# Kernel tuning notes

Measured on AMD Instinct MI355X. Metric: run time of the kernel, lower is better.

## Reference

```python
import jax, jax.numpy as jnp
import numpy as np

B, C, L, M, EMB, HID = 32, 64, 8192, 32, 256, 64

def setup_inputs() -> dict:
    key = jax.random.key(0)
    ks = jax.random.split(key, 14)
    s_w = 1.0 / (C * C)
    s_a = 1.0 / EMB
    return {
        "x": jax.random.normal(ks[0], (B, C, L), jnp.float32),
        "emb": jax.random.normal(ks[1], (B, EMB), jnp.float32),
        "weights_pos": s_w * jax.random.normal(ks[2], (C, C, M, 2), jnp.float32),
        "weights_neg": s_w * jax.random.normal(ks[3], (C, C, M, 2), jnp.float32),
        "A_real_pos": s_a * jax.random.normal(ks[4], (M, EMB), jnp.float32),
        "A_imag_pos": s_a * jax.random.normal(ks[5], (M, EMB), jnp.float32),
        "A_real_neg": s_a * jax.random.normal(ks[6], (M, EMB), jnp.float32),
        "A_imag_neg": s_a * jax.random.normal(ks[7], (M, EMB), jnp.float32),
        "tm_w1": 0.05 * jax.random.normal(ks[8], (HID, EMB), jnp.float32),
        "tm_b1": jnp.zeros((HID,), jnp.float32),
        "tm_w2": 0.05 * jax.random.normal(ks[9], (2 * C, HID), jnp.float32),
        "tm_b2": jnp.zeros((2 * C,), jnp.float32),
        "lin_w": 0.05 * jax.random.normal(ks[10], (C, C), jnp.float32),
        "lin_b": jnp.zeros((C,), jnp.float32),
    }

def reference(x, emb, weights_pos, weights_neg, A_real_pos, A_imag_pos,
              A_real_neg, A_imag_neg, tm_w1, tm_b1, tm_w2, tm_b2, lin_w, lin_b):
    b, c, l = x.shape
    m = weights_pos.shape[2]
    k = l // 2 + 1
    # ---- SpectralConv1d branch ----
    x_ft = jnp.fft.rfft(x, norm="ortho")  # [B,C,K] complex
    wp = weights_pos[..., 0] + 1j * weights_pos[..., 1]  # [Ci,Co,M]
    wn = weights_neg[..., 0] + 1j * weights_neg[..., 1]
    phi_p = (emb @ A_real_pos.T) + 1j * (emb @ A_imag_pos.T)  # [B,M]
    phi_n = (emb @ A_real_neg.T) + 1j * (emb @ A_imag_neg.T)
    out_pos = jnp.einsum("bim,iom->bom", x_ft[:, :, :m], wp) * phi_p[:, None, :]
    out_neg = jnp.einsum("bim,iom->bom", x_ft[:, :, k - m:], wn) * phi_n[:, None, :]
    out_ft = jnp.zeros((b, c, k), dtype=x_ft.dtype)
    out_ft = out_ft.at[:, :, :m].set(out_pos).at[:, :, k - m:].set(out_neg)
    x1 = jnp.fft.irfft(out_ft, n=l, norm="ortho")  # [B,C,L]
    # ---- Conv1DTime branch (FiLM-style) ----
    h = jax.nn.silu(emb @ tm_w1.T + tm_b1)          # [B,HID]
    gb = h @ tm_w2.T + tm_b2                         # [B,2C]
    gamma, beta = gb[:, :c], gb[:, c:]
    xl = jnp.einsum("bcl,oc->bol", x, lin_w) + lin_b[None, :, None]
    x2 = xl * (1.0 + gamma[:, :, None]) + beta[:, :, None]
    return jax.nn.silu(x1 + x2)
```

## Files before the change

### kernel.cpp

```cpp
#include <hip/hip_runtime.h>
#include <math.h>

#define L_ 8192
#define EMB_ 256
#define HID_ 64

typedef __attribute__((ext_vector_type(8))) short bf16x8;
typedef __attribute__((ext_vector_type(4))) float f32x4;
typedef __attribute__((ext_vector_type(4))) int i32x4;

#define OFF_TFB  0
#define OFF_TLB  262144
#define OFF_AFB  524288
#define OFF_XFRP 917504
#define OFF_B2   3014656
#define OFF_PHI  3016704
#define OFF_GB   3020800

__device__ inline int pkbf(float a, float b) {
    int r;
    asm volatile("v_cvt_pk_bf16_f32 %0, %1, %2" : "=v"(r) : "v"(a), "v"(b));
    return r;
}
__device__ inline bf16x8 asbf(i32x4 v) { union { i32x4 i; bf16x8 h; } u; u.i = v; return u.h; }
#define MFMA(A,B,C) __builtin_amdgcn_mfma_f32_16x16x32_bf16((A),(B),(C),0,0,0)

__device__ inline ushort f2bf(float v) {
    unsigned b = __float_as_uint(v);
    return (ushort)((b + 0x7FFFu + ((b >> 16) & 1u)) >> 16);
}
__device__ inline float bf2f(ushort h) { return __uint_as_float(((unsigned)h) << 16); }
__device__ inline float hwsin(float rev) { float r; asm("v_sin_f32 %0, %1" : "=v"(r) : "v"(rev)); return r; }
__device__ inline float hwcos(float rev) { float r; asm("v_cos_f32 %0, %1" : "=v"(r) : "v"(rev)); return r; }

__global__ __launch_bounds__(256) void k_init(ushort* __restrict__ TLB, ushort* __restrict__ TFB,
        const float* __restrict__ emb,
        const float* __restrict__ Arp, const float* __restrict__ Aip,
        const float* __restrict__ Arn, const float* __restrict__ Ain, float* __restrict__ phi,
        const float* __restrict__ w1, const float* __restrict__ b1,
        const float* __restrict__ w2, const float* __restrict__ b2, float* __restrict__ gb) {
    int bid = blockIdx.x;
    if (bid < 4096) {
        int idx = bid * 256 + threadIdx.x;
        int f, l; ushort* dst;
        if (idx < 524288) {
            int u = idx;
            int e = u & 7, lane = (u >> 3) & 63, ct = (u >> 9) & 3, kstep = u >> 11;
            l = kstep * 32 + ((lane >> 4) << 3) + e;
            f = ct * 16 + (lane & 15);
            dst = TLB + u;
        } else {
            int u = idx - 524288;
            int e = u & 7, lane = (u >> 3) & 63, ts = (u >> 9) & 1, lt = u >> 10;
            l = lt * 16 + (lane & 15);
            f = ts * 32 + ((lane >> 4) << 3) + e;
            dst = TFB + u;
        }
        int fr = f & 31; bool sinp = (f & 32) != 0;
        int r = (fr * l) & (L_ - 1);
        float rev = (float)r * (1.0f / (float)L_);
        float v = sinp ? hwsin(rev) : hwcos(rev);
        *dst = f2bf(v);
    } else if (bid < 4112) {
        int tid = (bid - 4096) * 256 + threadIdx.x;
        int b = tid >> 7;
        int mm = (tid >> 2) & 31;
        int cmp = tid & 3;
        const float* A = (cmp == 0) ? Arp : (cmp == 1) ? Aip : (cmp == 2) ? Arn : Ain;
        const float4* e4 = (const float4*)(emb + b * EMB_);
        const float4* a4 = (const float4*)(A + mm * EMB_);
        float acc = 0.f;
        for (int q = 0; q < EMB_ / 4; ++q) {
            float4 ev = e4[q], av = a4[q];
            acc += ev.x * av.x + ev.y * av.y + ev.z * av.z + ev.w * av.w;
        }
        phi[tid] = acc;
    } else {
        __shared__ float h[HID_];
        int b = bid - 4112, t = threadIdx.x;
        if (t < HID_) {
            const float4* e4 = (const float4*)(emb + b * EMB_);
            const float4* w4 = (const float4*)(w1 + t * EMB_);
            float acc = b1[t];
            for (int q = 0; q < EMB_ / 4; ++q) {
                float4 ev = e4[q], wv = w4[q];
                acc += ev.x * wv.x + ev.y * wv.y + ev.z * wv.z + ev.w * wv.w;
            }
            h[t] = acc / (1.f + expf(-acc));
        }
        __syncthreads();
        if (t < 128) {
            float g = b2[t];
            const float4* h4 = (const float4*)h;
            const float4* w4 = (const float4*)(w2 + t * HID_);
            for (int q = 0; q < HID_ / 4; ++q) {
                float4 hv = h4[q], wv = w4[q];
                g += hv.x * wv.x + hv.y * wv.y + hv.z * wv.z + hv.w * wv.w;
            }
            if (t < 64) gb[(b * 64 + t) * 2 + 0] = 1.f + g;
            else        gb[(b * 64 + (t - 64)) * 2 + 1] = g;
        }
    }
}

__global__ __launch_bounds__(256) void k_dft(const float* __restrict__ x,
        const ushort* __restrict__ TLB, float* __restrict__ xfrp) {
    __shared__ float sP[4][16][132];
    int stripe = blockIdx.x >> 3;
    int lseg = blockIdx.x & 7;
    int w = threadIdx.x >> 6;
    int lane = threadIdx.x & 63;
    int row = lane & 15, koff = (lane >> 4) << 3;
    int r0 = stripe * 16;
    int kb0 = lseg * 1024 + w * 256;

    f32x4 acc[8];
    #pragma unroll
    for (int i = 0; i < 8; ++i) acc[i] = (f32x4){0.f, 0.f, 0.f, 0.f};

    const float* ap = x + (size_t)(r0 + row) * L_ + kb0 + koff;
    const i32x4* tb = (const i32x4*)TLB;
    int tbase = (kb0 >> 5) * 256 + lane;
    const i32x4 SM = {(int)0x80000000, (int)0x80000000, (int)0x80000000, (int)0x80000000};

    float4 xa0 = *(const float4*)(ap);
    float4 xc0 = *(const float4*)(ap + 4);
    float4 xa1 = *(const float4*)(ap + 32);
    float4 xc1 = *(const float4*)(ap + 36);
    float4 xa2 = *(const float4*)(ap + 64);
    float4 xc2 = *(const float4*)(ap + 68);
    i32x4 t0 = tb[tbase], t1 = tb[tbase + 64], t2 = tb[tbase + 128], t3 = tb[tbase + 192];
    for (int ks = 0; ks < 8; ++ks) {
        float4 nxa = {0,0,0,0}, nxc = {0,0,0,0};
        i32x4 n0 = t0, n1 = t1, n2 = t2, n3 = t3;
        if (ks < 5) {
            nxa = *(const float4*)(ap + (ks + 3) * 32);
            nxc = *(const float4*)(ap + (ks + 3) * 32 + 4);
        }
        if (ks < 7) {
            int ti = tbase + (ks + 1) * 256;
            n0 = tb[ti]; n1 = tb[ti + 64]; n2 = tb[ti + 128]; n3 = tb[ti + 192];
        }
        int h0 = pkbf(xa0.x, xa0.y), h1 = pkbf(xa0.z, xa0.w);
        int h2 = pkbf(xc0.x, xc0.y), h3 = pkbf(xc0.z, xc0.w);
        bf16x8 AH = asbf((i32x4){h0, h1, h2, h3});
        acc[0] = MFMA(AH, asbf(t0), acc[0]); acc[4] = MFMA(AH, asbf(t0 ^ SM), acc[4]);
        acc[1] = MFMA(AH, asbf(t1), acc[1]); acc[5] = MFMA(AH, asbf(t1 ^ SM), acc[5]);
        acc[2] = MFMA(AH, asbf(t2), acc[2]); acc[6] = MFMA(AH, asbf(t2 ^ SM), acc[6]);
        acc[3] = MFMA(AH, asbf(t3), acc[3]); acc[7] = MFMA(AH, asbf(t3 ^ SM), acc[7]);
        xa0 = xa1; xc0 = xc1; xa1 = xa2; xc1 = xc2; xa2 = nxa; xc2 = nxc;
        t0 = n0; t1 = n1; t2 = n2; t3 = n3;
    }
    int crow = (lane >> 4) << 2;
    int ccol = lane & 15;
    #pragma unroll
    for (int ct = 0; ct < 8; ++ct)
        #pragma unroll
        for (int r = 0; r < 4; ++r)
            sP[w][crow + r][ct * 16 + ccol] = acc[ct][r];
    __syncthreads();
    #pragma unroll
    for (int i = 0; i < 8; ++i) {
        int e = threadIdx.x + 256 * i;
        int rr = e & 15, cc = e >> 4;
        float s = sP[0][rr][cc] + sP[1][rr][cc] + sP[2][rr][cc] + sP[3][rr][cc];
        xfrp[((size_t)(lseg * 128 + cc)) * 2048 + r0 + rr] = s;
    }
}

__global__ __launch_bounds__(256) void k_mix(const float* __restrict__ xfrt,
        const float* __restrict__ wpos, const float* __restrict__ wneg,
        const float* __restrict__ phi, const float* __restrict__ lw,
        const float* __restrict__ lb, const float* __restrict__ gb,
        ushort* __restrict__ afb, float* __restrict__ bias2) {
    int bi = blockIdx.x;
    int tid = threadIdx.x;
    if (bi >= 128) {
        int b = bi - 128;
        ushort* dst = afb + (size_t)b * 24576;
        #pragma unroll
        for (int j = 0; j < 16; ++j) {
            int u = tid + 256 * j;
            int e = u & 7, lane = (u >> 3) & 63, mt = (u >> 9) & 3, ks2 = u >> 11;
            int c = mt * 16 + (lane & 15);
            int kk = ((lane >> 4) << 3) + e;
            float v = lw[c * 64 + ks2 * 32 + kk] * gb[(b * 64 + c) * 2];
            ushort hi = f2bf(v);
            int base = (((4 + ks2) * 4 + mt) * 64 + lane) * 16;
            dst[base + e] = hi;
            dst[base + 8 + e] = f2bf(v - bf2f(hi));
        }
        if (tid < 64) {
            float g1 = gb[(b * 64 + tid) * 2], be = gb[(b * 64 + tid) * 2 + 1];
            bias2[b * 64 + tid] = lb[tid] * g1 + be;
        }
        return;
    }
    __shared__ float sW[64][64][2];
    __shared__ float sXr[16][64], sXi[16][64];
    int bh = bi & 1, side = (bi >> 1) & 1, mm = bi >> 2;
    int slot = side ? (31 - mm) : mm;
    int colR = side ? (64 + slot) : mm;
    int colI = side ? (96 + slot) : (32 + mm);

    const float* W = side ? wneg : wpos;
    #pragma unroll
    for (int j = 0; j < 16; ++j) {
        int fidx = tid + 256 * j;
        int i = fidx >> 6, o = fidx & 63;
        float2 wv = *(const float2*)&W[(size_t)(i * 64 + o) * 64 + mm * 2];
        sW[i][o][0] = wv.x;
        sW[i][o][1] = wv.y;
    }
    {
        const float4* pR = (const float4*)(xfrt + (size_t)colR * 2048 + bh * 1024);
        const float4* pI = (const float4*)(xfrt + (size_t)colI * 2048 + bh * 1024);
        float4 aR = {0, 0, 0, 0}, aI = {0, 0, 0, 0};
        #pragma unroll
        for (int s = 0; s < 8; ++s) {
            float4 vR = pR[(size_t)s * 65536 + tid];
            float4 vI = pI[(size_t)s * 65536 + tid];
            aR.x += vR.x; aR.y += vR.y; aR.z += vR.z; aR.w += vR.w;
            aI.x += vI.x; aI.y += vI.y; aI.z += vI.z; aI.w += vI.w;
        }
        if (!side) { aI.x = -aI.x; aI.y = -aI.y; aI.z = -aI.z; aI.w = -aI.w; }
        *(float4*)&sXr[tid >> 4][(tid & 15) * 4] = aR;
        *(float4*)&sXi[tid >> 4][(tid & 15) * 4] = aI;
    }
    __syncthreads();

    int o = tid & 63, bg = tid >> 6;
    const float invL = 1.f / (float)L_;
    float fac = (slot == 0) ? invL : 2.f * invL;
    int comp = side ? 2 : 0;
    int e = slot & 7, kgrp = slot >> 3;
    int mt = o >> 4, lane = kgrp * 16 + (o & 15);
    #pragma unroll
    for (int bl = 0; bl < 4; ++bl) {
        int b_local = bg * 4 + bl;
        int b = bh * 16 + b_local;
        float sre = 0.f, sim = 0.f;
        #pragma unroll 16
        for (int i = 0; i < 64; ++i) {
            float wr = sW[i][o][0], wi = sW[i][o][1];
            float xr = sXr[b_local][i], xi = sXi[b_local][i];
            sre += xr * wr - xi * wi;
            sim += xr * wi + xi * wr;
        }
        const float* ph = &phi[(b * 32 + mm) * 4 + (side ? 2 : 0)];
        float phr = ph[0], phim = ph[1];
        float Pre = sre * phr - sim * phim;
        float Pim = sre * phim + sim * phr;
        float a = fac * Pre;
        float bcoef = (slot == 0) ? 0.f : (side ? 2.f * invL * Pim : -2.f * invL * Pim);
        ushort* dst = afb + (size_t)b * 24576;
        ushort hiA = f2bf(a);
        int baseA = ((comp * 4 + mt) * 64 + lane) * 16;
        dst[baseA + e] = hiA;
        dst[baseA + 8 + e] = f2bf(a - bf2f(hiA));
        ushort hiB = f2bf(bcoef);
        int baseB = (((comp + 1) * 4 + mt) * 64 + lane) * 16;
        dst[baseB + e] = hiB;
        dst[baseB + 8 + e] = f2bf(bcoef - bf2f(hiB));
    }
}

__global__ __launch_bounds__(256, 4) void k_fuse(const float* __restrict__ x,
        const ushort* __restrict__ TFB, const ushort* __restrict__ AFB,
        const float* __restrict__ bias2, float* __restrict__ out) {
    int b = blockIdx.x >> 6, lt = blockIdx.x & 63;
    int w = threadIdx.x >> 6, lane = threadIdx.x & 63;
    int col = lane & 15, kgrp = lane >> 4;
    int lbase = lt * 128 + w * 32;
    int lt0 = lbase >> 4;
    const i32x4* tb = (const i32x4*)TFB;
    const i32x4* ab = (const i32x4*)AFB + (size_t)b * 3072;

    f32x4 acc[4][2];
    #pragma unroll
    for (int i = 0; i < 4; ++i)
        #pragma unroll
        for (int j = 0; j < 2; ++j) acc[i][j] = (f32x4){0.f, 0.f, 0.f, 0.f};

    int sm = (col & 1) ? (int)0x80008000 : 0;
    i32x4 SM = {sm, sm, sm, sm};

    auto tpart = [&](int ts) {
        i32x4 bh[2];
        #pragma unroll
        for (int nj = 0; nj < 2; ++nj)
            bh[nj] = tb[((lt0 + nj) * 2 + ts) * 64 + lane];
        #pragma unroll
        for (int mt = 0; mt < 4; ++mt) {
            i32x4 ah0 = ab[((ts * 4 + mt) * 64 + lane) * 2];
            i32x4 ah1 = ab[(((2 + ts) * 4 + mt) * 64 + lane) * 2];
            bf16x8 AH0 = asbf(ah0), AH1 = asbf(ah1);
            #pragma unroll
            for (int nj = 0; nj < 2; ++nj) {
                acc[mt][nj] = MFMA(AH0, asbf(bh[nj]), acc[mt][nj]);
                acc[mt][nj] = MFMA(AH1, asbf(bh[nj] ^ SM), acc[mt][nj]);
            }
        }
    };
    auto xissue = [&](int ts, float xv[2][8]) {
        #pragma unroll
        for (int nj = 0; nj < 2; ++nj) {
            const float* xp = x + (size_t)(b * 64 + ts * 32 + kgrp * 8) * L_ + lbase + nj * 16 + col;
            #pragma unroll
            for (int e = 0; e < 8; ++e) xv[nj][e] = xp[(size_t)e * L_];
        }
    };
    auto xpart = [&](int ts, float xv[2][8]) {
        #pragma unroll
        for (int nj = 0; nj < 2; ++nj) {
            int h0 = pkbf(xv[nj][0], xv[nj][1]), h1 = pkbf(xv[nj][2], xv[nj][3]);
            int h2 = pkbf(xv[nj][4], xv[nj][5]), h3 = pkbf(xv[nj][6], xv[nj][7]);
            bf16x8 XH = asbf((i32x4){h0, h1, h2, h3});
            #pragma unroll
            for (int mt = 0; mt < 4; ++mt) {
                i32x4 ah = ab[(((4 + ts) * 4 + mt) * 64 + lane) * 2];
                acc[mt][nj] = MFMA(asbf(ah), XH, acc[mt][nj]);
            }
        }
    };

    float xva[2][8], xvb[2][8];
    xissue(0, xva);
    tpart(0);
    xissue(1, xvb);
    xpart(0, xva);
    tpart(1);
    xpart(1, xvb);

    #pragma unroll
    for (int mt = 0; mt < 4; ++mt) {
        #pragma unroll
        for (int r = 0; r < 4; ++r) {
            int c = mt * 16 + kgrp * 4 + r;
            float bias = bias2[b * 64 + c];
            float* op = out + (size_t)(b * 64 + c) * L_ + lbase + col;
            #pragma unroll
            for (int nj = 0; nj < 2; ++nj) {
                float v = acc[mt][nj][r] + bias;
                op[nj * 16] = v / (1.f + __expf(-v));
            }
        }
    }
}

extern "C" void kernel_launch(void* const* d_in, const int* in_sizes, int n_in,
                              void* d_out, int out_size, void* d_ws, size_t ws_size,
                              hipStream_t stream) {
    const float* x    = (const float*)d_in[0];
    const float* emb  = (const float*)d_in[1];
    const float* wpos = (const float*)d_in[2];
    const float* wneg = (const float*)d_in[3];
    const float* Arp  = (const float*)d_in[4];
    const float* Aip  = (const float*)d_in[5];
    const float* Arn  = (const float*)d_in[6];
    const float* Ain  = (const float*)d_in[7];
    const float* w1   = (const float*)d_in[8];
    const float* b1   = (const float*)d_in[9];
    const float* w2   = (const float*)d_in[10];
    const float* b2   = (const float*)d_in[11];
    const float* lw   = (const float*)d_in[12];
    const float* lb   = (const float*)d_in[13];
    float* out = (float*)d_out;
    float* ws = (float*)d_ws;
    ushort* TFB  = (ushort*)(ws + OFF_TFB);
    ushort* TLB  = (ushort*)(ws + OFF_TLB);
    ushort* AFB  = (ushort*)(ws + OFF_AFB);
    float*  XFRP = ws + OFF_XFRP;
    float*  B2   = ws + OFF_B2;
    float*  PHI  = ws + OFF_PHI;
    float*  GB   = ws + OFF_GB;

    hipLaunchKernelGGL(k_init,  dim3(4144), dim3(256), 0, stream,
                       TLB, TFB, emb, Arp, Aip, Arn, Ain, PHI, w1, b1, w2, b2, GB);
    hipLaunchKernelGGL(k_dft,   dim3(1024), dim3(256), 0, stream, x, TLB, XFRP);
    hipLaunchKernelGGL(k_mix,   dim3(160),  dim3(256), 0, stream, XFRP, wpos, wneg, PHI,
                       lw, lb, GB, AFB, B2);
    hipLaunchKernelGGL(k_fuse,  dim3(2048), dim3(256), 0, stream, x, TFB, AFB, B2, out);
}
```

Measured before the change: 72.82 us.

## Split k_mix batch across more blocks, unroll DFT loop, reorder fuse x loads

k_mix now splits the batch into four groups of 8 instead of two groups of 16, so it launches 256 mixing blocks plus 32 affine blocks instead of 128 plus 32. This gives more parallelism on a small-grid kernel at the cost of reloading the weight tile in more blocks. The k_dft k-step loop is fully unrolled. In k_fuse the lambdas become macros, both x loads are issued before any MFMA work, and the occupancy hint drops from 4 to 3 blocks per CU to allow more registers for the earlier prefetch.

```diff
diff --git a/kernel.cpp b/kernel.cpp
--- a/kernel.cpp
+++ b/kernel.cpp
@@ -130,6 +130,7 @@
     float4 xa2 = *(const float4*)(ap + 64);
     float4 xc2 = *(const float4*)(ap + 68);
     i32x4 t0 = tb[tbase], t1 = tb[tbase + 64], t2 = tb[tbase + 128], t3 = tb[tbase + 192];
+    #pragma unroll
     for (int ks = 0; ks < 8; ++ks) {
         float4 nxa = {0,0,0,0}, nxc = {0,0,0,0};
         i32x4 n0 = t0, n1 = t1, n2 = t2, n3 = t3;
@@ -175,8 +176,8 @@
         ushort* __restrict__ afb, float* __restrict__ bias2) {
     int bi = blockIdx.x;
     int tid = threadIdx.x;
-    if (bi >= 128) {
-        int b = bi - 128;
+    if (bi >= 256) {
+        int b = bi - 256;
         ushort* dst = afb + (size_t)b * 24576;
         #pragma unroll
         for (int j = 0; j < 16; ++j) {
@@ -197,8 +198,8 @@
         return;
     }
     __shared__ float sW[64][64][2];
-    __shared__ float sXr[16][64], sXi[16][64];
-    int bh = bi & 1, side = (bi >> 1) & 1, mm = bi >> 2;
+    __shared__ float sXr[8][64], sXi[8][64];
+    int bh = bi & 3, side = (bi >> 2) & 1, mm = bi >> 3;
     int slot = side ? (31 - mm) : mm;
     int colR = side ? (64 + slot) : mm;
     int colI = side ? (96 + slot) : (32 + mm);
@@ -213,19 +214,19 @@
         sW[i][o][1] = wv.y;
     }
     {
-        const float4* pR = (const float4*)(xfrt + (size_t)colR * 2048 + bh * 1024);
-        const float4* pI = (const float4*)(xfrt + (size_t)colI * 2048 + bh * 1024);
-        float4 aR = {0, 0, 0, 0}, aI = {0, 0, 0, 0};
+        const float2* pR = (const float2*)(xfrt + (size_t)colR * 2048 + bh * 512);
+        const float2* pI = (const float2*)(xfrt + (size_t)colI * 2048 + bh * 512);
+        float2 aR = {0, 0}, aI = {0, 0};
         #pragma unroll
         for (int s = 0; s < 8; ++s) {
-            float4 vR = pR[(size_t)s * 65536 + tid];
-            float4 vI = pI[(size_t)s * 65536 + tid];
-            aR.x += vR.x; aR.y += vR.y; aR.z += vR.z; aR.w += vR.w;
-            aI.x += vI.x; aI.y += vI.y; aI.z += vI.z; aI.w += vI.w;
-        }
-        if (!side) { aI.x = -aI.x; aI.y = -aI.y; aI.z = -aI.z; aI.w = -aI.w; }
-        *(float4*)&sXr[tid >> 4][(tid & 15) * 4] = aR;
-        *(float4*)&sXi[tid >> 4][(tid & 15) * 4] = aI;
+            float2 vR = pR[(size_t)s * 131072 + tid];
+            float2 vI = pI[(size_t)s * 131072 + tid];
+            aR.x += vR.x; aR.y += vR.y;
+            aI.x += vI.x; aI.y += vI.y;
+        }
+        if (!side) { aI.x = -aI.x; aI.y = -aI.y; }
+        *(float2*)&sXr[tid >> 5][(tid & 31) * 2] = aR;
+        *(float2*)&sXi[tid >> 5][(tid & 31) * 2] = aI;
     }
     __syncthreads();
 
@@ -236,9 +237,9 @@
     int e = slot & 7, kgrp = slot >> 3;
     int mt = o >> 4, lane = kgrp * 16 + (o & 15);
     #pragma unroll
-    for (int bl = 0; bl < 4; ++bl) {
-        int b_local = bg * 4 + bl;
-        int b = bh * 16 + b_local;
+    for (int bl = 0; bl < 2; ++bl) {
+        int b_local = bg * 2 + bl;
+        int b = bh * 8 + b_local;
         float sre = 0.f, sim = 0.f;
         #pragma unroll 16
         for (int i = 0; i < 64; ++i) {
@@ -265,7 +266,48 @@
     }
 }
 
-__global__ __launch_bounds__(256, 4) void k_fuse(const float* __restrict__ x,
+#define XISSUE(ts, xv)                                                                   \
+    _Pragma("unroll")                                                                    \
+    for (int nj = 0; nj < 2; ++nj) {                                                     \
+        const float* xp = x + (size_t)(b * 64 + (ts) * 32 + kgrp * 8) * L_               \
+                            + lbase + nj * 16 + col;                                     \
+        _Pragma("unroll")                                                                \
+        for (int e = 0; e < 8; ++e) xv[nj][e] = xp[(size_t)e * L_];                      \
+    }
+
+#define TPART(ts)                                                                        \
+    {                                                                                    \
+        i32x4 bh_[2];                                                                    \
+        _Pragma("unroll")                                                                \
+        for (int nj = 0; nj < 2; ++nj)                                                   \
+            bh_[nj] = tb[((lt0 + nj) * 2 + (ts)) * 64 + lane];                           \
+        _Pragma("unroll")                                                                \
+        for (int mt = 0; mt < 4; ++mt) {                                                 \
+            i32x4 ah0 = ab[(((ts) * 4 + mt) * 64 + lane) * 2];                           \
+            i32x4 ah1 = ab[(((2 + (ts)) * 4 + mt) * 64 + lane) * 2];                     \
+            bf16x8 AH0 = asbf(ah0), AH1 = asbf(ah1);                                     \
+            _Pragma("unroll")                                                            \
+            for (int nj = 0; nj < 2; ++nj) {                                             \
+                acc[mt][nj] = MFMA(AH0, asbf(bh_[nj]), acc[mt][nj]);                     \
+                acc[mt][nj] = MFMA(AH1, asbf(bh_[nj] ^ SM), acc[mt][nj]);                \
+            }                                                                            \
+        }                                                                                \
+    }
+
+#define XPART(ts, xv)                                                                    \
+    _Pragma("unroll")                                                                    \
+    for (int nj = 0; nj < 2; ++nj) {                                                     \
+        int h0 = pkbf(xv[nj][0], xv[nj][1]), h1 = pkbf(xv[nj][2], xv[nj][3]);            \
+        int h2 = pkbf(xv[nj][4], xv[nj][5]), h3 = pkbf(xv[nj][6], xv[nj][7]);            \
+        bf16x8 XH = asbf((i32x4){h0, h1, h2, h3});                                       \
+        _Pragma("unroll")                                                                \
+        for (int mt = 0; mt < 4; ++mt) {                                                 \
+            i32x4 ah = ab[(((4 + (ts)) * 4 + mt) * 64 + lane) * 2];                      \
+            acc[mt][nj] = MFMA(asbf(ah), XH, acc[mt][nj]);                               \
+        }                                                                                \
+    }
+
+__global__ __launch_bounds__(256, 3) void k_fuse(const float* __restrict__ x,
         const ushort* __restrict__ TFB, const ushort* __restrict__ AFB,
         const float* __restrict__ bias2, float* __restrict__ out) {
     int b = blockIdx.x >> 6, lt = blockIdx.x & 63;
@@ -285,52 +327,13 @@
     int sm = (col & 1) ? (int)0x80008000 : 0;
     i32x4 SM = {sm, sm, sm, sm};
 
-    auto tpart = [&](int ts) {
-        i32x4 bh[2];
-        #pragma unroll
-        for (int nj = 0; nj < 2; ++nj)
-            bh[nj] = tb[((lt0 + nj) * 2 + ts) * 64 + lane];
-        #pragma unroll
-        for (int mt = 0; mt < 4; ++mt) {
-            i32x4 ah0 = ab[((ts * 4 + mt) * 64 + lane) * 2];
-            i32x4 ah1 = ab[(((2 + ts) * 4 + mt) * 64 + lane) * 2];
-            bf16x8 AH0 = asbf(ah0), AH1 = asbf(ah1);
-            #pragma unroll
-            for (int nj = 0; nj < 2; ++nj) {
-                acc[mt][nj] = MFMA(AH0, asbf(bh[nj]), acc[mt][nj]);
-                acc[mt][nj] = MFMA(AH1, asbf(bh[nj] ^ SM), acc[mt][nj]);
-            }
-        }
-    };
-    auto xissue = [&](int ts, float xv[2][8]) {
-        #pragma unroll
-        for (int nj = 0; nj < 2; ++nj) {
-            const float* xp = x + (size_t)(b * 64 + ts * 32 + kgrp * 8) * L_ + lbase + nj * 16 + col;
-            #pragma unroll
-            for (int e = 0; e < 8; ++e) xv[nj][e] = xp[(size_t)e * L_];
-        }
-    };
-    auto xpart = [&](int ts, float xv[2][8]) {
-        #pragma unroll
-        for (int nj = 0; nj < 2; ++nj) {
-            int h0 = pkbf(xv[nj][0], xv[nj][1]), h1 = pkbf(xv[nj][2], xv[nj][3]);
-            int h2 = pkbf(xv[nj][4], xv[nj][5]), h3 = pkbf(xv[nj][6], xv[nj][7]);
-            bf16x8 XH = asbf((i32x4){h0, h1, h2, h3});
-            #pragma unroll
-            for (int mt = 0; mt < 4; ++mt) {
-                i32x4 ah = ab[(((4 + ts) * 4 + mt) * 64 + lane) * 2];
-                acc[mt][nj] = MFMA(asbf(ah), XH, acc[mt][nj]);
-            }
-        }
-    };
-
     float xva[2][8], xvb[2][8];
-    xissue(0, xva);
-    tpart(0);
-    xissue(1, xvb);
-    xpart(0, xva);
-    tpart(1);
-    xpart(1, xvb);
+    XISSUE(0, xva)
+    XISSUE(1, xvb)
+    TPART(0)
+    XPART(0, xva)
+    TPART(1)
+    XPART(1, xvb)
 
     #pragma unroll
     for (int mt = 0; mt < 4; ++mt) {
@@ -378,7 +381,7 @@
     hipLaunchKernelGGL(k_init,  dim3(4144), dim3(256), 0, stream,
                        TLB, TFB, emb, Arp, Aip, Arn, Ain, PHI, w1, b1, w2, b2, GB);
     hipLaunchKernelGGL(k_dft,   dim3(1024), dim3(256), 0, stream, x, TLB, XFRP);
-    hipLaunchKernelGGL(k_mix,   dim3(160),  dim3(256), 0, stream, XFRP, wpos, wneg, PHI,
+    hipLaunchKernelGGL(k_mix,   dim3(288),  dim3(256), 0, stream, XFRP, wpos, wneg, PHI,
                        lw, lb, GB, AFB, B2);
     hipLaunchKernelGGL(k_fuse,  dim3(2048), dim3(256), 0, stream, x, TFB, AFB, B2, out);
 }
```

Result: faster. 69.11 us (-5.1%).
